# Kernel tuning notes

Hardware: AMD Instinct MI355X
Metric: run time of the kernel (lower is better)

Reference implementation:

```python
import jax, jax.numpy as jnp
import numpy as np

NH = 25            # nHidden
NS = 20            # nStep (MPC horizon)
DT = 1.0 / 60.0    # del_t
EPS = 1e-4
PQ = 5.0           # terminal cost weight
QV = 200.0         # velocity cost weight
QA = 1.0           # control cost weight
BATCH = 131072
D = NH + 2         # augmented state dim


def setup_inputs() -> dict:
    key = jax.random.key(0)
    k1, k2, k3, k4, k5 = jax.random.split(key, 5)
    x = jax.random.normal(k1, (BATCH, NH), jnp.float32)
    gripper_p = jax.random.normal(k2, (BATCH,), jnp.float32)
    gripper_v = jax.random.normal(k3, (BATCH,), jnp.float32)
    # learned parameters of the module
    Af = jax.random.uniform(k4, (NH, 1), jnp.float32)               # feature->position coupling column
    Lq = jnp.tril(jax.random.uniform(k5, (NH, NH), jnp.float32))    # Cholesky-style factor of Q0
    return {"x": x, "gripper_p": gripper_p, "gripper_v": gripper_v, "Af": Af, "Lq": Lq}


def _build_system(Af, Lq):
    """Assemble the (batch-shared) MPC matrices: Q_final, p_final, S_, T_."""
    eyeD = jnp.eye(D, dtype=Af.dtype)
    # A0 = [[I, 0, Af], [0 .. 0, [1 dt; 0 1]]]
    top = jnp.concatenate([jnp.eye(NH, dtype=Af.dtype), jnp.zeros((NH, 1), Af.dtype), Af], axis=1)
    ap = jnp.concatenate([jnp.zeros((2, NH), Af.dtype),
                          jnp.array([[1.0, DT], [0.0, 1.0]], Af.dtype)], axis=1)
    A0 = jnp.concatenate([top, ap], axis=0)                                   # [D, D]
    B0 = jnp.concatenate([jnp.zeros((NH, 1), Af.dtype),
                          jnp.array([[0.5 * DT * DT], [DT]], Af.dtype)], axis=0)  # [D, 1]
    # stage cost Q0 (padded with [0 0; 0 Qv] block)
    Q0 = Lq @ Lq.T + EPS * jnp.eye(NH, dtype=Af.dtype)
    Q0f = (jnp.zeros((D, D), Af.dtype)
           .at[:NH, :NH].set(Q0)
           .at[NH:, NH:].set(jnp.array([[0.0, 0.0], [0.0, QV]], Af.dtype)))
    # powers A0^0..A0^NS (small fixed loop, NS=20)
    pows = [eyeD]
    for _ in range(NS):
        pows.append(pows[-1] @ A0)
    P = jnp.stack(pows)                    # [NS+1, D, D]
    T_ = P[1:].reshape(NS * D, D)          # stacked A0^1..A0^NS
    # S_ block (r,c) = A0^(r-c) @ B0 for c<=r (block lower-triangular), else 0
    SB = P @ B0                            # [NS+1, D, 1]
    r = jnp.arange(NS)
    diff = r[:, None] - r[None, :]         # [NS, NS]
    Sblk = jnp.where((diff >= 0)[:, :, None, None], SB[jnp.clip(diff, 0)], 0.0)  # [NS, NS, D, 1]
    S_ = Sblk.transpose(0, 2, 1, 3).reshape(NS * D, NS)
    # block-diagonal Q (last block scaled by Pq)
    Qblocks = jnp.concatenate([jnp.tile(Q0f[None], (NS - 1, 1, 1)), PQ * Q0f[None]], axis=0)
    Qd = jnp.zeros((NS, D, NS, D), Af.dtype).at[r, :, r, :].set(Qblocks).reshape(NS * D, NS * D)
    QS = Qd @ S_                                                       # [NS*D, NS]
    Q_final = 2.0 * (QA * jnp.eye(NS, dtype=Af.dtype) + S_.T @ QS) + EPS * jnp.eye(NS, dtype=Af.dtype)
    p_final = 2.0 * (T_.T @ QS)                                        # [D, NS]
    return Q_final, p_final, S_, T_


def reference(x, gripper_p, gripper_v, Af, Lq):
    nB = x.shape[0]
    Q_final, p_final, S_, T_ = _build_system(Af, Lq)
    x0 = jnp.concatenate([x, gripper_p[:, None], gripper_v[:, None]], axis=1)  # [B, D]
    p = x0 @ p_final                                                           # [B, NS]
    # QP with G=0, h=0 (trivially satisfied) and no equality constraints ->
    # unconstrained minimizer: u = -Q_final^{-1} p
    u = -jnp.linalg.solve(Q_final, p.T).T                                      # [B, NS]
    x_predict = u @ S_.T + x0 @ T_.T                                           # [B, NS*D]
    # output selector picks the gripper position entry (index NH) of each block
    return x_predict.reshape(nB, NS, D)[:, :, NH]                              # [B, NS]
```

## Files before the change

### kernel.cpp

```cpp
#include <hip/hip_runtime.h>

#define NHID 25
#define NSTEP 20
#define DT_ (1.0/60.0)
#define EPS_ 1e-4
#define PQ_ 5.0
#define QV_ 200.0
#define QA_ 1.0

__global__ __launch_bounds__(64) void setup_kernel(
    const float* __restrict__ Af, const float* __restrict__ Lq,
    float* __restrict__ C)
{
    __shared__ float  Afs[NHID];
    __shared__ double wv_[NHID];
    __shared__ double uv_[NHID];
    __shared__ double alpha_s;
    __shared__ double zs[2][NSTEP];

    const int t = threadIdx.x;
    const double dt = DT_;

    if (t < NHID) Afs[t] = Af[t];
    __syncthreads();

    if (t < NHID) {
        double acc = 0.0;
        for (int i = t; i < NHID; ++i)
            acc += (double)Lq[i * NHID + t] * (double)Afs[i];
        wv_[t] = acc;
    }
    __syncthreads();
    if (t < NHID) {
        double acc = EPS_ * (double)Afs[t];
        for (int j = 0; j <= t; ++j)
            acc += (double)Lq[t * NHID + j] * wv_[j];
        uv_[t] = acc;
    }
    __syncthreads();
    if (t == 0) {
        double a = 0.0;
        for (int i = 0; i < NHID; ++i) a += (double)Afs[i] * uv_[i];
        alpha_s = a;
    }
    __syncthreads();
    const double alpha = alpha_s;

    double row[NSTEP + 2];
    #pragma unroll
    for (int c = 0; c < NSTEP; ++c) {
        int m0 = (t > c) ? t : c;
        double s = 0.0;
        for (int rr = m0; rr < NSTEP; ++rr) {
            double wr = (rr == NSTEP - 1) ? PQ_ : 1.0;
            s += wr * ((double)(rr - t) * (double)(rr - c) * alpha + QV_);
        }
        row[c] = 2.0 * dt * dt * s + ((t == c) ? (2.0 * QA_ + EPS_) : 0.0);
    }
    {
        double s20 = 0.0, s21 = 0.0;
        for (int rr = t; rr < NSTEP; ++rr) {
            double wr = (rr == NSTEP - 1) ? PQ_ : 1.0;
            s20 += wr * (double)(rr - t);
            s21 += wr * ((double)(rr + 1) * (double)(rr - t) * alpha + QV_);
        }
        row[NSTEP]     = s20;
        row[NSTEP + 1] = s21;
    }

    #pragma unroll
    for (int piv = 0; piv < NSTEP; ++piv) {
        double pr[NSTEP + 2];
        #pragma unroll
        for (int c = piv; c < NSTEP + 2; ++c)
            pr[c] = __shfl(row[c], piv, 64);
        __builtin_amdgcn_sched_barrier(0);
        double pinv = 1.0 / pr[piv];
        double f = row[piv] * pinv;
        #pragma unroll
        for (int c = piv; c < NSTEP + 2; ++c) {
            double nv = row[c] - f * pr[c];
            row[c] = (t == piv) ? (pr[c] * pinv) : nv;
        }
    }
    if (t < NSTEP) { zs[0][t] = row[NSTEP]; zs[1][t] = row[NSTEP + 1]; }
    __syncthreads();

    if (t < NHID) C[t] = (float)uv_[t];
    if (t < NSTEP) {
        const double hdt2 = 0.5 * dt * dt;
        double bacc = 0.0, gacc = 0.0;
        for (int c = 0; c <= t; ++c) {
            double ssel = hdt2 + (double)(t - c) * dt * dt;
            bacc += zs[0][c] * ssel;
            gacc += zs[1][c] * ssel;
        }
        C[32 + t] = (float)(-2.0 * dt * bacc);
        C[64 + t] = (float)((double)(t + 1) * dt - 2.0 * dt * gacc);
    }
}

__global__ __launch_bounds__(256) void mpc_main(
    const float* __restrict__ x, const float* __restrict__ gp,
    const float* __restrict__ gv, const float* __restrict__ C,
    float* __restrict__ out)
{
    __shared__ float xs[256 * NHID];
    __shared__ float us[NHID];
    __shared__ float bs[NSTEP];
    __shared__ float gs[NSTEP];
    const int t = threadIdx.x;
    const size_t b0 = (size_t)blockIdx.x * 256;

    if (t < NHID)                us[t] = C[t];
    else if (t >= 32 && t < 52)  bs[t - 32] = C[t];
    else if (t >= 64 && t < 84)  gs[t - 64] = C[t];

    {
        const float4* xsrc = (const float4*)(x + b0 * NHID);
        float4* xdst = (float4*)xs;
        #pragma unroll
        for (int i = 0; i < 7; ++i) {
            int idx = t + 256 * i;
            if (idx < 1600) xdst[idx] = xsrc[idx];
        }
    }
    const float p = gp[b0 + t];
    const float v = gv[b0 + t];
    __syncthreads();

    const float* xr = xs + t * NHID;
    float tb = 0.0f;
    #pragma unroll
    for (int i = 0; i < NHID; ++i)
        tb = fmaf(xr[i], us[i], tb);

    float4* o4 = (float4*)(out + (b0 + t) * NSTEP);
    #pragma unroll
    for (int q = 0; q < 5; ++q) {
        float4 r;
        r.x = fmaf(tb, bs[4*q+0], fmaf(v, gs[4*q+0], p));
        r.y = fmaf(tb, bs[4*q+1], fmaf(v, gs[4*q+1], p));
        r.z = fmaf(tb, bs[4*q+2], fmaf(v, gs[4*q+2], p));
        r.w = fmaf(tb, bs[4*q+3], fmaf(v, gs[4*q+3], p));
        o4[q] = r;
    }
}

extern "C" void kernel_launch(void* const* d_in, const int* in_sizes, int n_in,
                              void* d_out, int out_size, void* d_ws, size_t ws_size,
                              hipStream_t stream) {
    const float* x  = (const float*)d_in[0];
    const float* gp = (const float*)d_in[1];
    const float* gv = (const float*)d_in[2];
    const float* Af = (const float*)d_in[3];
    const float* Lq = (const float*)d_in[4];
    float* out = (float*)d_out;
    float* C   = (float*)d_ws;

    const int B = in_sizes[1];
    hipLaunchKernelGGL(setup_kernel, dim3(1), dim3(64), 0, stream, Af, Lq, C);
    hipLaunchKernelGGL(mpc_main, dim3(B / 256), dim3(256), 0, stream,
                       x, gp, gv, C, out);
}
```

Baseline: 95.47 us.

## Fuse setup solve into main kernel with per-block fp32 recomputation

Drops the separate single-block setup kernel. Every block of the main kernel now recomputes the batch-shared coefficients (Lq·Af products, the 20x20 Gauss-Jordan solve via shuffles) in fp32 and keeps them in shared memory. This saves one kernel launch and the serial dependency on the one-block setup. In exchange, 512 blocks each repeat the redundant serial solve with several extra barriers. Switching from double to float risks accuracy in the elimination.

```diff
diff --git a/kernel.cpp b/kernel.cpp
--- a/kernel.cpp
+++ b/kernel.cpp
@@ -2,120 +2,33 @@
 
 #define NHID 25
 #define NSTEP 20
-#define DT_ (1.0/60.0)
-#define EPS_ 1e-4
-#define PQ_ 5.0
-#define QV_ 200.0
-#define QA_ 1.0
+#define DT_ (1.0f/60.0f)
+#define EPS_ 1e-4f
+#define PQ_ 5.0f
+#define QV_ 200.0f
+#define QA_ 1.0f
 
-__global__ __launch_bounds__(64) void setup_kernel(
-    const float* __restrict__ Af, const float* __restrict__ Lq,
-    float* __restrict__ C)
+__global__ __launch_bounds__(256) void mpc_fused(
+    const float* __restrict__ x, const float* __restrict__ gp,
+    const float* __restrict__ gv, const float* __restrict__ Af,
+    const float* __restrict__ Lq, float* __restrict__ out)
 {
-    __shared__ float  Afs[NHID];
-    __shared__ double wv_[NHID];
-    __shared__ double uv_[NHID];
-    __shared__ double alpha_s;
-    __shared__ double zs[2][NSTEP];
+    __shared__ float xs[256 * NHID];
+    __shared__ float Lqs[NHID * NHID];
+    __shared__ float Afs[NHID];
+    __shared__ float wv_[NHID];
+    __shared__ float us[NHID];
+    __shared__ float alpha_s;
+    __shared__ float zsh[2][NSTEP];
+    __shared__ float bs[NSTEP];
+    __shared__ float gs[NSTEP];
 
     const int t = threadIdx.x;
-    const double dt = DT_;
+    const size_t b0 = (size_t)blockIdx.x * 256;
+    const float dt = DT_;
 
     if (t < NHID) Afs[t] = Af[t];
-    __syncthreads();
-
-    if (t < NHID) {
-        double acc = 0.0;
-        for (int i = t; i < NHID; ++i)
-            acc += (double)Lq[i * NHID + t] * (double)Afs[i];
-        wv_[t] = acc;
-    }
-    __syncthreads();
-    if (t < NHID) {
-        double acc = EPS_ * (double)Afs[t];
-        for (int j = 0; j <= t; ++j)
-            acc += (double)Lq[t * NHID + j] * wv_[j];
-        uv_[t] = acc;
-    }
-    __syncthreads();
-    if (t == 0) {
-        double a = 0.0;
-        for (int i = 0; i < NHID; ++i) a += (double)Afs[i] * uv_[i];
-        alpha_s = a;
-    }
-    __syncthreads();
-    const double alpha = alpha_s;
-
-    double row[NSTEP + 2];
-    #pragma unroll
-    for (int c = 0; c < NSTEP; ++c) {
-        int m0 = (t > c) ? t : c;
-        double s = 0.0;
-        for (int rr = m0; rr < NSTEP; ++rr) {
-            double wr = (rr == NSTEP - 1) ? PQ_ : 1.0;
-            s += wr * ((double)(rr - t) * (double)(rr - c) * alpha + QV_);
-        }
-        row[c] = 2.0 * dt * dt * s + ((t == c) ? (2.0 * QA_ + EPS_) : 0.0);
-    }
-    {
-        double s20 = 0.0, s21 = 0.0;
-        for (int rr = t; rr < NSTEP; ++rr) {
-            double wr = (rr == NSTEP - 1) ? PQ_ : 1.0;
-            s20 += wr * (double)(rr - t);
-            s21 += wr * ((double)(rr + 1) * (double)(rr - t) * alpha + QV_);
-        }
-        row[NSTEP]     = s20;
-        row[NSTEP + 1] = s21;
-    }
-
-    #pragma unroll
-    for (int piv = 0; piv < NSTEP; ++piv) {
-        double pr[NSTEP + 2];
-        #pragma unroll
-        for (int c = piv; c < NSTEP + 2; ++c)
-            pr[c] = __shfl(row[c], piv, 64);
-        __builtin_amdgcn_sched_barrier(0);
-        double pinv = 1.0 / pr[piv];
-        double f = row[piv] * pinv;
-        #pragma unroll
-        for (int c = piv; c < NSTEP + 2; ++c) {
-            double nv = row[c] - f * pr[c];
-            row[c] = (t == piv) ? (pr[c] * pinv) : nv;
-        }
-    }
-    if (t < NSTEP) { zs[0][t] = row[NSTEP]; zs[1][t] = row[NSTEP + 1]; }
-    __syncthreads();
-
-    if (t < NHID) C[t] = (float)uv_[t];
-    if (t < NSTEP) {
-        const double hdt2 = 0.5 * dt * dt;
-        double bacc = 0.0, gacc = 0.0;
-        for (int c = 0; c <= t; ++c) {
-            double ssel = hdt2 + (double)(t - c) * dt * dt;
-            bacc += zs[0][c] * ssel;
-            gacc += zs[1][c] * ssel;
-        }
-        C[32 + t] = (float)(-2.0 * dt * bacc);
-        C[64 + t] = (float)((double)(t + 1) * dt - 2.0 * dt * gacc);
-    }
-}
-
-__global__ __launch_bounds__(256) void mpc_main(
-    const float* __restrict__ x, const float* __restrict__ gp,
-    const float* __restrict__ gv, const float* __restrict__ C,
-    float* __restrict__ out)
-{
-    __shared__ float xs[256 * NHID];
-    __shared__ float us[NHID];
-    __shared__ float bs[NSTEP];
-    __shared__ float gs[NSTEP];
-    const int t = threadIdx.x;
-    const size_t b0 = (size_t)blockIdx.x * 256;
-
-    if (t < NHID)                us[t] = C[t];
-    else if (t >= 32 && t < 52)  bs[t - 32] = C[t];
-    else if (t >= 64 && t < 84)  gs[t - 64] = C[t];
-
+    for (int i = t; i < NHID * NHID; i += 256) Lqs[i] = Lq[i];
     {
         const float4* xsrc = (const float4*)(x + b0 * NHID);
         float4* xdst = (float4*)xs;
@@ -127,6 +40,82 @@
     }
     const float p = gp[b0 + t];
     const float v = gv[b0 + t];
+    __syncthreads();
+
+    if (t < NHID) {
+        float acc = 0.0f;
+        for (int i = t; i < NHID; ++i)
+            acc = fmaf(Lqs[i * NHID + t], Afs[i], acc);
+        wv_[t] = acc;
+    }
+    __syncthreads();
+    if (t < NHID) {
+        float acc = EPS_ * Afs[t];
+        for (int j = 0; j <= t; ++j)
+            acc = fmaf(Lqs[t * NHID + j], wv_[j], acc);
+        us[t] = acc;
+    }
+    __syncthreads();
+    if (t == 0) {
+        float a = 0.0f;
+        for (int i = 0; i < NHID; ++i) a = fmaf(Afs[i], us[i], a);
+        alpha_s = a;
+    }
+    __syncthreads();
+
+    if (t < 64) {
+        const float alpha = alpha_s;
+        float row[NSTEP + 2];
+        #pragma unroll
+        for (int c = 0; c < NSTEP; ++c) {
+            int m0 = (t > c) ? t : c;
+            float s = 0.0f;
+            for (int rr = m0; rr < NSTEP; ++rr) {
+                float wr = (rr == NSTEP - 1) ? PQ_ : 1.0f;
+                s = fmaf(wr, fmaf((float)(rr - t) * (float)(rr - c), alpha, QV_), s);
+            }
+            row[c] = 2.0f * dt * dt * s + ((t == c) ? (2.0f * QA_ + EPS_) : 0.0f);
+        }
+        {
+            float s20 = 0.0f, s21 = 0.0f;
+            for (int rr = t; rr < NSTEP; ++rr) {
+                float wr = (rr == NSTEP - 1) ? PQ_ : 1.0f;
+                s20 += wr * (float)(rr - t);
+                s21 = fmaf(wr, fmaf((float)(rr + 1) * (float)(rr - t), alpha, QV_), s21);
+            }
+            row[NSTEP]     = s20;
+            row[NSTEP + 1] = s21;
+        }
+        #pragma unroll
+        for (int piv = 0; piv < NSTEP; ++piv) {
+            float pr[NSTEP + 2];
+            #pragma unroll
+            for (int c = piv; c < NSTEP + 2; ++c)
+                pr[c] = __shfl(row[c], piv, 64);
+            __builtin_amdgcn_sched_barrier(0);
+            float pinv = 1.0f / pr[piv];
+            float f = row[piv] * pinv;
+            #pragma unroll
+            for (int c = piv; c < NSTEP + 2; ++c) {
+                float nv = fmaf(-f, pr[c], row[c]);
+                row[c] = (t == piv) ? (pr[c] * pinv) : nv;
+            }
+        }
+        if (t < NSTEP) { zsh[0][t] = row[NSTEP]; zsh[1][t] = row[NSTEP + 1]; }
+    }
+    __syncthreads();
+
+    if (t < NSTEP) {
+        const float hdt2 = 0.5f * dt * dt;
+        float bacc = 0.0f, gacc = 0.0f;
+        for (int c = 0; c <= t; ++c) {
+            float ssel = fmaf((float)(t - c), dt * dt, hdt2);
+            bacc = fmaf(zsh[0][c], ssel, bacc);
+            gacc = fmaf(zsh[1][c], ssel, gacc);
+        }
+        bs[t] = -2.0f * dt * bacc;
+        gs[t] = fmaf((float)(t + 1), dt, -2.0f * dt * gacc);
+    }
     __syncthreads();
 
     const float* xr = xs + t * NHID;
@@ -156,10 +145,8 @@
     const float* Af = (const float*)d_in[3];
     const float* Lq = (const float*)d_in[4];
     float* out = (float*)d_out;
-    float* C   = (float*)d_ws;
 
     const int B = in_sizes[1];
-    hipLaunchKernelGGL(setup_kernel, dim3(1), dim3(64), 0, stream, Af, Lq, C);
-    hipLaunchKernelGGL(mpc_main, dim3(B / 256), dim3(256), 0, stream,
-                       x, gp, gv, C, out);
+    hipLaunchKernelGGL(mpc_fused, dim3(B / 256), dim3(256), 0, stream,
+                       x, gp, gv, Af, Lq, out);
 }
```

Result: faster. 90.28 us (-5.4%).
